# Performance work log

Hardware: AMD Instinct MI355X
Metric: run time of the kernel (lower is better)

The kernel has to match this reference:

```python
import jax, jax.numpy as jnp
import numpy as np

B, S, D = 2, 2048, 1024
NUM_HEAD = 8
HEAD_SIZE = D // NUM_HEAD


def setup_inputs() -> dict:
    key = jax.random.key(0)
    ks = jax.random.split(key, 10)
    scale = 1.0 / np.sqrt(D)
    inp = {
        "q": jax.random.normal(ks[0], (B, S, D), dtype=jnp.float32),
        "k": jax.random.normal(ks[1], (B, S, D), dtype=jnp.float32),
        "v": jax.random.normal(ks[2], (B, S, D), dtype=jnp.float32),
        "mask": jax.random.bernoulli(ks[3], 0.1, (B, 1, S, S)),
        "Wq": jax.random.normal(ks[4], (D, D), dtype=jnp.float32) * scale,
        "bq": jnp.zeros((D,), dtype=jnp.float32),
        "Wk": jax.random.normal(ks[5], (D, D), dtype=jnp.float32) * scale,
        "bk": jnp.zeros((D,), dtype=jnp.float32),
        "Wv": jax.random.normal(ks[6], (D, D), dtype=jnp.float32) * scale,
        "bv": jnp.zeros((D,), dtype=jnp.float32),
    }
    return inp


def _split_heads(x):
    # [B,S,D] -> [B,H,S,Hd]
    b, s, _ = x.shape
    return x.reshape(b, s, NUM_HEAD, HEAD_SIZE).transpose(0, 2, 1, 3)


def reference(q, k, v, mask, Wq, bq, Wk, bk, Wv, bv):
    Q = _split_heads(q @ Wq + bq)
    K = _split_heads(k @ Wk + bk)
    V = _split_heads(v @ Wv + bv)
    # scores [B,H,S,S]; NB: mask applied BEFORE scaling, as in the original
    QK = jnp.einsum("bhqd,bhkd->bhqk", Q, K)
    QK = jnp.where(mask, jnp.float32(-1e6), QK)
    QK = QK / jnp.float32(np.sqrt(HEAD_SIZE))
    attn = jax.nn.softmax(QK, axis=-1)  # dropout is identity in eval mode
    ctx = jnp.einsum("bhqk,bhkd->bhqd", attn, V)
    out = ctx.transpose(0, 2, 1, 3).reshape(q.shape[0], q.shape[1], D)
    return out
```

## Files before the change

kernel.cpp:

```cpp
#include <hip/hip_runtime.h>

typedef __bf16 bf16;
typedef __attribute__((ext_vector_type(8))) __bf16 bf16x8;
typedef __attribute__((ext_vector_type(4))) __bf16 bf16x4;
typedef __attribute__((ext_vector_type(4))) float f32x4;
typedef __attribute__((ext_vector_type(4))) float fvec4;

#define NB 2
#define SEQ 2048
#define DM 1024
#define NH 8
#define HD 128

#define QSCL (0.08838834764831845f * 1.4426950408889634f)

#define AS1 __attribute__((address_space(1)))
#define AS3 __attribute__((address_space(3)))

__global__ __launch_bounds__(256) void prep_kernel(
    const float* __restrict__ qi, const float* __restrict__ ki,
    const float* __restrict__ vi,
    const float* __restrict__ Wq, const float* __restrict__ Wk,
    const float* __restrict__ Wv,
    const unsigned int* __restrict__ mask32,
    bf16* __restrict__ Xc, bf16* __restrict__ Wt,
    unsigned int* __restrict__ flag)
{
    const int z   = blockIdx.y;
    const int tid = threadIdx.x;
    __shared__ __align__(16) bf16 tile[64][80];
    __shared__ unsigned int sred[256];

    if (z < 3) {
        const float* src = (z == 0) ? qi : (z == 1) ? ki : vi;
        bf16* dst = Xc + (size_t)z * ((size_t)NB * SEQ * DM);
        const size_t base = (size_t)blockIdx.x * 4096 + (size_t)tid * 16;
        fvec4 f[4];
        #pragma unroll
        for (int j = 0; j < 4; j++)
            f[j] = *(const fvec4*)(src + base + j * 4);
        bf16x8 h0, h1;
        #pragma unroll
        for (int e = 0; e < 8; e++) {
            h0[e] = (bf16)f[e >> 2][e & 3];
            h1[e] = (bf16)f[2 + (e >> 2)][e & 3];
        }
        *(bf16x8*)(dst + base)     = h0;
        *(bf16x8*)(dst + base + 8) = h1;
    } else if (z < 6) {
        if (blockIdx.x >= 256) return;
        const float* W = (z == 3) ? Wq : (z == 4) ? Wk : Wv;
        bf16* dst = Wt + (size_t)(z - 3) * ((size_t)DM * DM);
        const float scl = (z == 3) ? QSCL : 1.0f;
        const int n0 = (blockIdx.x & 15) * 64;
        const int k0 = (blockIdx.x >> 4) * 64;
        #pragma unroll
        for (int p = 0; p < 4; p++) {
            const int r = p * 16 + (tid >> 4);
            const int c = (tid & 15) * 4;
            const fvec4 wv = *(const fvec4*)(W + (size_t)(k0 + r) * DM + n0 + c);
            #pragma unroll
            for (int j = 0; j < 4; j++)
                tile[c + j][r] = (bf16)(wv[j] * scl);
        }
        __syncthreads();
        #pragma unroll
        for (int p = 0; p < 2; p++) {
            const int row = p * 32 + (tid >> 3);
            const int ch  = tid & 7;
            const bf16x8 hv = *(const bf16x8*)(&tile[row][ch * 8]);
            *(bf16x8*)(dst + (size_t)(n0 + row) * DM + k0 + ch * 8) = hv;
        }
    } else {
        if (blockIdx.x != 0) return;
        unsigned int f = 0;
        for (int i = tid; i < 1024; i += 256) {
            const unsigned int w2 = mask32[i];
            if ((w2 & 0xFEFEFEFEu) == 0u && (w2 & 0xFFFFFF00u) != 0u) f = 1;
        }
        sred[tid] = f;
        __syncthreads();
        if (tid == 0) {
            unsigned int r = 0;
            for (int i = 0; i < 256; i++) r |= sred[i];
            *flag = r;
        }
    }
}

__global__ __launch_bounds__(256) void proj_kernel(
    const bf16* __restrict__ Xc, const bf16* __restrict__ Wt,
    const float* __restrict__ bq, const float* __restrict__ bk,
    const float* __restrict__ bv,
    bf16* __restrict__ Qo, bf16* __restrict__ Ko, bf16* __restrict__ Vto,
    const void* __restrict__ mask, const unsigned int* __restrict__ flag,
    unsigned long long* __restrict__ bits)
{
    __shared__ __align__(16) bf16 As[2][128 * 64];
    __shared__ __align__(16) bf16 Bs[2][128 * 64];

    const int pz = blockIdx.z;
    const int tid = threadIdx.x;

    if (pz == 3) {
        const bool bytem = (*flag & 1u) != 0;
        const int wid = blockIdx.y * 8 + blockIdx.x;
        const int t   = wid * 256 + tid;
        unsigned short* const bits16o = (unsigned short*)bits;
        #pragma unroll 2
        for (int it = 0; it < 8; ++it) {
            const size_t e0 = ((size_t)it * 65536 + t) * 16;
            unsigned int b16 = 0;
            if (bytem) {
                const uint4 wv = *(const uint4*)((const unsigned char*)mask + e0);
                const unsigned int wd[4] = {wv.x, wv.y, wv.z, wv.w};
                #pragma unroll
                for (int j = 0; j < 4; j++) {
                    b16 |= ((wd[j] & 0x000000FFu) ? 1u : 0u) << (4 * j + 0);
                    b16 |= ((wd[j] & 0x0000FF00u) ? 1u : 0u) << (4 * j + 1);
                    b16 |= ((wd[j] & 0x00FF0000u) ? 1u : 0u) << (4 * j + 2);
                    b16 |= ((wd[j] & 0xFF000000u) ? 1u : 0u) << (4 * j + 3);
                }
            } else {
                const unsigned int* mw = (const unsigned int*)mask + e0;
                #pragma unroll
                for (int j = 0; j < 4; j++) {
                    const uint4 wv = *(const uint4*)(mw + 4 * j);
                    b16 |= (wv.x ? 1u : 0u) << (4 * j + 0);
                    b16 |= (wv.y ? 1u : 0u) << (4 * j + 1);
                    b16 |= (wv.z ? 1u : 0u) << (4 * j + 2);
                    b16 |= (wv.w ? 1u : 0u) << (4 * j + 3);
                }
            }
            bits16o[e0 >> 4] = (unsigned short)b16;
        }
        return;
    }

    const bf16* X  = Xc + (size_t)pz * ((size_t)NB * SEQ * DM);
    const bf16* Bt = Wt + (size_t)pz * ((size_t)DM * DM);
    const float* bias = (pz == 0) ? bq : (pz == 1) ? bk : bv;
    const float bscl  = (pz == 0) ? QSCL : 1.0f;
    bf16* dst = (pz == 0) ? Qo : (pz == 1) ? Ko : Vto;

    const int lane = tid & 63;
    const int w    = tid >> 6;
    const int q16  = lane >> 4;
    const int l15  = lane & 15;

    const int m0 = blockIdx.y * 128;
    const int n0 = blockIdx.x * 128;
    const int wm = (w >> 1) * 64;
    const int wn = (w & 1) * 64;

    auto stage = [&](int buf, int k0) {
        #pragma unroll
        for (int i = 0; i < 4; i++) {
            const int c   = i * 256 + tid;
            const int row = c >> 3;
            const int cir = c & 7;
            const bf16* src =
                X + (size_t)(m0 + row) * DM + k0 + ((cir ^ (row & 7)) << 3);
            __builtin_amdgcn_global_load_lds(
                (const AS1 void*)src,
                (AS3 void*)(&As[buf][c * 8]),
                16, 0, 0);
        }
        #pragma unroll
        for (int i = 0; i < 4; i++) {
            const int c   = i * 256 + tid;
            const int row = c >> 3;
            const int cir = c & 7;
            const bf16* src =
                Bt + (size_t)(n0 + row) * DM + k0 + ((cir ^ (row & 7)) << 3);
            __builtin_amdgcn_global_load_lds(
                (const AS1 void*)src,
                (AS3 void*)(&Bs[buf][c * 8]),
                16, 0, 0);
        }
    };

    f32x4 acc[4][4] = {};
    stage(0, 0);
    __syncthreads();
    int cur = 0;

    for (int kt = 0; kt < DM / 64; ++kt) {
        if (kt + 1 < DM / 64) stage(cur ^ 1, (kt + 1) * 64);
        const bf16* Asb = &As[cur][0];
        const bf16* Bsb = &Bs[cur][0];
        #pragma unroll
        for (int c2 = 0; c2 < 2; c2++) {
            bf16x8 af[4], bfr[4];
            #pragma unroll
            for (int mi = 0; mi < 4; mi++) {
                const int row = wm + mi * 16 + l15;
                af[mi] = *(const bf16x8*)(
                    Asb + row * 64 + (((c2 * 4 + q16) ^ (row & 7)) << 3));
            }
            #pragma unroll
            for (int ni = 0; ni < 4; ni++) {
                const int row = wn + ni * 16 + l15;
                bfr[ni] = *(const bf16x8*)(
                    Bsb + row * 64 + (((c2 * 4 + q16) ^ (row & 7)) << 3));
            }
            #pragma unroll
            for (int mi = 0; mi < 4; mi++)
                #pragma unroll
                for (int ni = 0; ni < 4; ni++)
                    acc[mi][ni] = __builtin_amdgcn_mfma_f32_16x16x32_bf16(
                        af[mi], bfr[ni], acc[mi][ni], 0, 0, 0);
        }
        __syncthreads();
        cur ^= 1;
    }

    float bias_v[4];
    #pragma unroll
    for (int ni = 0; ni < 4; ni++)
        bias_v[ni] = bias[n0 + wn + ni * 16 + l15];

    #pragma unroll
    for (int mi = 0; mi < 4; mi++) {
        #pragma unroll
        for (int ni = 0; ni < 4; ni++) {
            const int n  = n0 + wn + ni * 16 + l15;
            const int h  = n >> 7;
            const int hd = n & (HD - 1);
            #pragma unroll
            for (int r = 0; r < 4; r++) {
                const int m = m0 + wm + mi * 16 + q16 * 4 + r;
                const int b = m >> 11;
                const int s = m & (SEQ - 1);
                const float val = acc[mi][ni][r] + bias_v[ni] * bscl;
                size_t idx;
                if (pz == 2)
                    idx = ((size_t)(b * NH + h) * HD + hd) * SEQ + s;
                else
                    idx = ((size_t)(b * NH + h) * SEQ + s) * HD + hd;
                dst[idx] = (bf16)val;
            }
        }
    }
}

__global__ __launch_bounds__(256) void attn_kernel(
    const bf16* __restrict__ Q, const bf16* __restrict__ K,
    const bf16* __restrict__ Vt, const unsigned int* __restrict__ maskbits,
    float* __restrict__ out)
{
    __shared__ __align__(16) bf16 Ks[2][64 * 128];
    __shared__ __align__(16) bf16 Vs[2][128 * 64];
    __shared__ __align__(16) bf16 Ps[4][16 * 72];

    const int tid  = threadIdx.x;
    const int lane = tid & 63;
    const int w    = tid >> 6;
    const int q16  = lane >> 4;
    const int l15  = lane & 15;
    const int l3   = l15 & 7;

    const int b  = blockIdx.z;
    const int h  = blockIdx.y;
    const int q0 = blockIdx.x * 64;
    const int bh = b * NH + h;

    const bf16* Qb = Q  + (size_t)bh * SEQ * HD;
    const bf16* Kb = K  + (size_t)bh * SEQ * HD;
    const bf16* Vb = Vt + (size_t)bh * HD * SEQ;
    const unsigned long long* mb64 =
        (const unsigned long long*)maskbits + (size_t)b * (SEQ * SEQ / 64);
    const int qbase = q0 + w * 16 + q16 * 4;
    const unsigned long long* mrow = mb64 + (size_t)qbase * (SEQ / 64);

    const int qrow_a = q0 + w * 16 + l15;
    bf16x8 qf[4];
    #pragma unroll
    for (int c = 0; c < 4; c++)
        qf[c] = *(const bf16x8*)(Qb + (size_t)qrow_a * HD + c * 32 + q16 * 8);

    f32x4 o[8] = {};
    float m_i[4], l_i[4];
    #pragma unroll
    for (int r = 0; r < 4; r++) { m_i[r] = -__builtin_inff(); l_i[r] = 0.f; }

    const float MASKV = -1.0e6f * QSCL;

    auto stage = [&](int buf, int k0) {
        bf16* kd = &Ks[buf][0];
        bf16* vd = &Vs[buf][0];
        #pragma unroll
        for (int i = 0; i < 4; i++) {
            const int c   = i * 256 + tid;
            const int row = c >> 4;
            const int cir = c & 15;
            const bf16* src =
                Kb + (size_t)(k0 + row) * HD + ((cir ^ (row & 7)) << 3);
            __builtin_amdgcn_global_load_lds(
                (const AS1 void*)src,
                (AS3 void*)(kd + c * 8),
                16, 0, 0);
        }
        #pragma unroll
        for (int i = 0; i < 4; i++) {
            const int c   = i * 256 + tid;
            const int d   = c >> 3;
            const int cir = c & 7;
            const bf16* src =
                Vb + (size_t)d * SEQ + k0 + ((cir ^ (d & 7)) << 3);
            __builtin_amdgcn_global_load_lds(
                (const AS1 void*)src,
                (AS3 void*)(vd + c * 8),
                16, 0, 0);
        }
    };

    unsigned long long mwn[4];
    stage(0, 0);
    #pragma unroll
    for (int r = 0; r < 4; r++) mwn[r] = mrow[(size_t)r * (SEQ / 64)];
    __syncthreads();

    bf16* Pw = &Ps[w][0];
    int cur = 0;

    for (int kt = 0; kt < SEQ / 64; ++kt) {
        unsigned long long mw[4];
        #pragma unroll
        for (int r = 0; r < 4; r++) mw[r] = mwn[r];

        if (kt + 1 < SEQ / 64) stage(cur ^ 1, (kt + 1) * 64);
        const int ktn = (kt + 1) & (SEQ / 64 - 1);
        #pragma unroll
        for (int r = 0; r < 4; r++)
            mwn[r] = mrow[(size_t)r * (SEQ / 64) + ktn];

        const bf16* Ksb = &Ks[cur][0];
        const bf16* Vsb = &Vs[cur][0];

        f32x4 sf[4] = {};
        #pragma unroll
        for (int c = 0; c < 4; c++) {
            #pragma unroll
            for (int nf = 0; nf < 4; nf++) {
                const bf16x8 kf = *(const bf16x8*)(
                    Ksb + (nf * 16 + l15) * 128 + (((c * 4 + q16) ^ l3) << 3));
                sf[nf] = __builtin_amdgcn_mfma_f32_16x16x32_bf16(
                    qf[c], kf, sf[nf], 0, 0, 0);
            }
        }

        #pragma unroll
        for (int nf = 0; nf < 4; nf++)
            #pragma unroll
            for (int r = 0; r < 4; r++) {
                const int mk = (int)((mw[r] >> (nf * 16 + l15)) & 1ull);
                sf[nf][r] = mk ? MASKV : sf[nf][r];
            }

        float alpha[4];
        bool need = false;
        #pragma unroll
        for (int r = 0; r < 4; r++) {
            float mx = fmaxf(fmaxf(sf[0][r], sf[1][r]),
                             fmaxf(sf[2][r], sf[3][r]));
            #pragma unroll
            for (int off = 1; off < 16; off <<= 1)
                mx = fmaxf(mx, __shfl_xor(mx, off, 16));
            const float mnew = fmaxf(m_i[r], mx);
            alpha[r] = __builtin_amdgcn_exp2f(m_i[r] - mnew);
            need |= (mnew > m_i[r]);
            m_i[r] = mnew;
            float ps = 0.f;
            #pragma unroll
            for (int nf = 0; nf < 4; nf++) {
                const float p = __builtin_amdgcn_exp2f(sf[nf][r] - mnew);
                sf[nf][r] = p;
                ps += p;
            }
            l_i[r] = l_i[r] * alpha[r] + ps;
        }

        if (__ballot(need)) {
            #pragma unroll
            for (int df = 0; df < 8; df++)
                #pragma unroll
                for (int r = 0; r < 4; r++)
                    o[df][r] *= alpha[r];
        }

        #pragma unroll
        for (int nf = 0; nf < 4; nf++)
            #pragma unroll
            for (int r = 0; r < 4; r++)
                Pw[(q16 * 4 + r) * 72 + nf * 16 + l15] = (bf16)sf[nf][r];

        bf16x8 pf[2];
        #pragma unroll
        for (int cc = 0; cc < 2; cc++)
            pf[cc] = *(const bf16x8*)(Pw + l15 * 72 + cc * 32 + q16 * 8);

        #pragma unroll
        for (int df = 0; df < 8; df++) {
            #pragma unroll
            for (int cc = 0; cc < 2; cc++) {
                const bf16x8 vf = *(const bf16x8*)(
                    Vsb + (df * 16 + l15) * 64 + (((cc * 4 + q16) ^ l3) << 3));
                o[df] = __builtin_amdgcn_mfma_f32_16x16x32_bf16(
                    pf[cc], vf, o[df], 0, 0, 0);
            }
        }

        __syncthreads();
        cur ^= 1;
    }

    #pragma unroll
    for (int r = 0; r < 4; r++) {
        float ls = l_i[r];
        #pragma unroll
        for (int off = 1; off < 16; off <<= 1)
            ls += __shfl_xor(ls, off, 16);
        l_i[r] = 1.0f / ls;
    }
    #pragma unroll
    for (int df = 0; df < 8; df++) {
        #pragma unroll
        for (int r = 0; r < 4; r++) {
            const int qr = q0 + w * 16 + q16 * 4 + r;
            out[((size_t)b * SEQ + qr) * DM + h * HD + df * 16 + l15] =
                o[df][r] * l_i[r];
        }
    }
}

extern "C" void kernel_launch(void* const* d_in, const int* in_sizes, int n_in,
                              void* d_out, int out_size, void* d_ws, size_t ws_size,
                              hipStream_t stream) {
    const float* q    = (const float*)d_in[0];
    const float* k    = (const float*)d_in[1];
    const float* v    = (const float*)d_in[2];
    const void*  mask = d_in[3];
    const float* Wq   = (const float*)d_in[4];
    const float* bq   = (const float*)d_in[5];
    const float* Wk   = (const float*)d_in[6];
    const float* bk   = (const float*)d_in[7];
    const float* Wv   = (const float*)d_in[8];
    const float* bv   = (const float*)d_in[9];
    float* out = (float*)d_out;

    char* ws = (char*)d_ws;
    unsigned long long* bits = (unsigned long long*)ws;
    const size_t bits_bytes = (size_t)NB * SEQ * SEQ / 8;
    unsigned int* flag = (unsigned int*)(ws + bits_bytes);
    bf16* Qp = (bf16*)(ws + bits_bytes + 256);
    bf16* Kp = Qp + (size_t)NB * SEQ * DM;
    bf16* Vp = Kp + (size_t)NB * SEQ * DM;
    bf16* Xc = Vp + (size_t)NB * SEQ * DM;
    bf16* Wt = Xc + (size_t)3 * NB * SEQ * DM;

    prep_kernel<<<dim3(1024, 7), 256, 0, stream>>>(
        q, k, v, Wq, Wk, Wv, (const unsigned int*)mask, Xc, Wt, flag);

    dim3 pgrid(DM / 128, (NB * SEQ) / 128, 4);
    proj_kernel<<<pgrid, 256, 0, stream>>>(Xc, Wt, bq, bk, bv, Qp, Kp, Vp,
                                           mask, flag, bits);

    dim3 agrid(SEQ / 64, NH, NB);
    attn_kernel<<<agrid, 256, 0, stream>>>(Qp, Kp, Vp,
                                           (const unsigned int*)bits, out);
}
```

Before: 278.8 us.

## Process 32 query rows per wave in attention to reuse K/V fragments

Each wave now handles two 16-row query tiles (128 queries per block instead of 64), so every K and V fragment read from LDS feeds two MFMAs. This halves the K/V global-to-LDS traffic per query and the LDS reads per MFMA. The mask-word prefetch for the next tile is dropped, and masks are now loaded at the top of each iteration. Register pressure roughly doubles for accumulators, and the grid shrinks to 256 blocks, which may underfill the 256 CUs.

Measured after the change: 305.3 us. 9.5% more time.

```diff
diff --git a/kernel.cpp b/kernel.cpp
--- a/kernel.cpp
+++ b/kernel.cpp
@@ -251,7 +251,7 @@
 {
     __shared__ __align__(16) bf16 Ks[2][64 * 128];
     __shared__ __align__(16) bf16 Vs[2][128 * 64];
-    __shared__ __align__(16) bf16 Ps[4][16 * 72];
+    __shared__ __align__(16) bf16 Ps[4][32 * 72];
 
     const int tid  = threadIdx.x;
     const int lane = tid & 63;
@@ -262,27 +262,35 @@
 
     const int b  = blockIdx.z;
     const int h  = blockIdx.y;
-    const int q0 = blockIdx.x * 64;
+    const int q0 = blockIdx.x * 128;
     const int bh = b * NH + h;
+    const int wrow = w * 32;
 
     const bf16* Qb = Q  + (size_t)bh * SEQ * HD;
     const bf16* Kb = K  + (size_t)bh * SEQ * HD;
     const bf16* Vb = Vt + (size_t)bh * HD * SEQ;
     const unsigned long long* mb64 =
         (const unsigned long long*)maskbits + (size_t)b * (SEQ * SEQ / 64);
-    const int qbase = q0 + w * 16 + q16 * 4;
-    const unsigned long long* mrow = mb64 + (size_t)qbase * (SEQ / 64);
-
-    const int qrow_a = q0 + w * 16 + l15;
-    bf16x8 qf[4];
-    #pragma unroll
-    for (int c = 0; c < 4; c++)
-        qf[c] = *(const bf16x8*)(Qb + (size_t)qrow_a * HD + c * 32 + q16 * 8);
-
-    f32x4 o[8] = {};
-    float m_i[4], l_i[4];
-    #pragma unroll
-    for (int r = 0; r < 4; r++) { m_i[r] = -__builtin_inff(); l_i[r] = 0.f; }
+    const unsigned long long* mrow[2];
+    #pragma unroll
+    for (int mi = 0; mi < 2; mi++)
+        mrow[mi] = mb64 +
+            (size_t)(q0 + wrow + mi * 16 + q16 * 4) * (SEQ / 64);
+
+    bf16x8 qf[2][4];
+    #pragma unroll
+    for (int mi = 0; mi < 2; mi++)
+        #pragma unroll
+        for (int c = 0; c < 4; c++)
+            qf[mi][c] = *(const bf16x8*)(
+                Qb + (size_t)(q0 + wrow + mi * 16 + l15) * HD + c * 32 + q16 * 8);
+
+    f32x4 o[2][8] = {};
+    float m_i[2][4], l_i[2][4];
+    #pragma unroll
+    for (int mi = 0; mi < 2; mi++)
+        #pragma unroll
+        for (int r = 0; r < 4; r++) { m_i[mi][r] = -__builtin_inff(); l_i[mi][r] = 0.f; }
 
     const float MASKV = -1.0e6f * QSCL;
 
@@ -315,90 +323,100 @@
         }
     };
 
-    unsigned long long mwn[4];
     stage(0, 0);
-    #pragma unroll
-    for (int r = 0; r < 4; r++) mwn[r] = mrow[(size_t)r * (SEQ / 64)];
     __syncthreads();
 
     bf16* Pw = &Ps[w][0];
     int cur = 0;
 
     for (int kt = 0; kt < SEQ / 64; ++kt) {
-        unsigned long long mw[4];
-        #pragma unroll
-        for (int r = 0; r < 4; r++) mw[r] = mwn[r];
+        unsigned long long mw[2][4];
+        #pragma unroll
+        for (int mi = 0; mi < 2; mi++)
+            #pragma unroll
+            for (int r = 0; r < 4; r++)
+                mw[mi][r] = mrow[mi][(size_t)r * (SEQ / 64) + kt];
 
         if (kt + 1 < SEQ / 64) stage(cur ^ 1, (kt + 1) * 64);
-        const int ktn = (kt + 1) & (SEQ / 64 - 1);
-        #pragma unroll
-        for (int r = 0; r < 4; r++)
-            mwn[r] = mrow[(size_t)r * (SEQ / 64) + ktn];
 
         const bf16* Ksb = &Ks[cur][0];
         const bf16* Vsb = &Vs[cur][0];
 
-        f32x4 sf[4] = {};
+        f32x4 sf[2][4] = {};
         #pragma unroll
         for (int c = 0; c < 4; c++) {
             #pragma unroll
             for (int nf = 0; nf < 4; nf++) {
                 const bf16x8 kf = *(const bf16x8*)(
                     Ksb + (nf * 16 + l15) * 128 + (((c * 4 + q16) ^ l3) << 3));
-                sf[nf] = __builtin_amdgcn_mfma_f32_16x16x32_bf16(
-                    qf[c], kf, sf[nf], 0, 0, 0);
-            }
-        }
-
-        #pragma unroll
-        for (int nf = 0; nf < 4; nf++)
+                #pragma unroll
+                for (int mi = 0; mi < 2; mi++)
+                    sf[mi][nf] = __builtin_amdgcn_mfma_f32_16x16x32_bf16(
+                        qf[mi][c], kf, sf[mi][nf], 0, 0, 0);
+            }
+        }
+
+        #pragma unroll
+        for (int mi = 0; mi < 2; mi++)
+            #pragma unroll
+            for (int nf = 0; nf < 4; nf++)
+                #pragma unroll
+                for (int r = 0; r < 4; r++) {
+                    const int mk = (int)((mw[mi][r] >> (nf * 16 + l15)) & 1ull);
+                    sf[mi][nf][r] = mk ? MASKV : sf[mi][nf][r];
+                }
+
+        float alpha[2][4];
+        bool need = false;
+        #pragma unroll
+        for (int mi = 0; mi < 2; mi++)
             #pragma unroll
             for (int r = 0; r < 4; r++) {
-                const int mk = (int)((mw[r] >> (nf * 16 + l15)) & 1ull);
-                sf[nf][r] = mk ? MASKV : sf[nf][r];
-            }
-
-        float alpha[4];
-        bool need = false;
-        #pragma unroll
-        for (int r = 0; r < 4; r++) {
-            float mx = fmaxf(fmaxf(sf[0][r], sf[1][r]),
-                             fmaxf(sf[2][r], sf[3][r]));
-            #pragma unroll
-            for (int off = 1; off < 16; off <<= 1)
-                mx = fmaxf(mx, __shfl_xor(mx, off, 16));
-            const float mnew = fmaxf(m_i[r], mx);
-            alpha[r] = __builtin_amdgcn_exp2f(m_i[r] - mnew);
-            need |= (mnew > m_i[r]);
-            m_i[r] = mnew;
-            float ps = 0.f;
-            #pragma unroll
-            for (int nf = 0; nf < 4; nf++) {
-                const float p = __builtin_amdgcn_exp2f(sf[nf][r] - mnew);
-                sf[nf][r] = p;
-                ps += p;
-            }
-            l_i[r] = l_i[r] * alpha[r] + ps;
-        }
+                float mx = fmaxf(fmaxf(sf[mi][0][r], sf[mi][1][r]),
+                                 fmaxf(sf[mi][2][r], sf[mi][3][r]));
+                #pragma unroll
+                for (int off = 1; off < 16; off <<= 1)
+                    mx = fmaxf(mx, __shfl_xor(mx, off, 16));
+                const float mnew = fmaxf(m_i[mi][r], mx);
+                alpha[mi][r] = __builtin_amdgcn_exp2f(m_i[mi][r] - mnew);
+                need |= (mnew > m_i[mi][r]);
+                m_i[mi][r] = mnew;
+                float ps = 0.f;
+                #pragma unroll
+                for (int nf = 0; nf < 4; nf++) {
+                    const float p = __builtin_amdgcn_exp2f(sf[mi][nf][r] - mnew);
+                    sf[mi][nf][r] = p;
+                    ps += p;
+                }
+                l_i[mi][r] = l_i[mi][r] * alpha[mi][r] + ps;
+            }
 
         if (__ballot(need)) {
             #pragma unroll
-            for (int df = 0; df < 8; df++)
+            for (int mi = 0; mi < 2; mi++)
+                #pragma unroll
+                for (int df = 0; df < 8; df++)
+                    #pragma unroll
+                    for (int r = 0; r < 4; r++)
+                        o[mi][df][r] *= alpha[mi][r];
+        }
+
+        #pragma unroll
+        for (int mi = 0; mi < 2; mi++)
+            #pragma unroll
+            for (int nf = 0; nf < 4; nf++)
                 #pragma unroll
                 for (int r = 0; r < 4; r++)
-                    o[df][r] *= alpha[r];
-        }
-
-        #pragma unroll
-        for (int nf = 0; nf < 4; nf++)
-            #pragma unroll
-            for (int r = 0; r < 4; r++)
-                Pw[(q16 * 4 + r) * 72 + nf * 16 + l15] = (bf16)sf[nf][r];
-
-        bf16x8 pf[2];
-        #pragma unroll
-        for (int cc = 0; cc < 2; cc++)
-            pf[cc] = *(const bf16x8*)(Pw + l15 * 72 + cc * 32 + q16 * 8);
+                    Pw[(mi * 16 + q16 * 4 + r) * 72 + nf * 16 + l15] =
+                        (bf16)sf[mi][nf][r];
+
+        bf16x8 pf[2][2];
+        #pragma unroll
+        for (int mi = 0; mi < 2; mi++)
+            #pragma unroll
+            for (int cc = 0; cc < 2; cc++)
+                pf[mi][cc] = *(const bf16x8*)(
+                    Pw + (mi * 16 + l15) * 72 + cc * 32 + q16 * 8);
 
         #pragma unroll
         for (int df = 0; df < 8; df++) {
@@ -406,8 +424,10 @@
             for (int cc = 0; cc < 2; cc++) {
                 const bf16x8 vf = *(const bf16x8*)(
                     Vsb + (df * 16 + l15) * 64 + (((cc * 4 + q16) ^ l3) << 3));
-                o[df] = __builtin_amdgcn_mfma_f32_16x16x32_bf16(
-                    pf[cc], vf, o[df], 0, 0, 0);
+                #pragma unroll
+                for (int mi = 0; mi < 2; mi++)
+                    o[mi][df] = __builtin_amdgcn_mfma_f32_16x16x32_bf16(
+                        pf[mi][cc], vf, o[mi][df], 0, 0, 0);
             }
         }
 
@@ -416,22 +436,26 @@
     }
 
     #pragma unroll
-    for (int r = 0; r < 4; r++) {
-        float ls = l_i[r];
-        #pragma unroll
-        for (int off = 1; off < 16; off <<= 1)
-            ls += __shfl_xor(ls, off, 16);
-        l_i[r] = 1.0f / ls;
-    }
-    #pragma unroll
-    for (int df = 0; df < 8; df++) {
+    for (int mi = 0; mi < 2; mi++)
         #pragma unroll
         for (int r = 0; r < 4; r++) {
-            const int qr = q0 + w * 16 + q16 * 4 + r;
-            out[((size_t)b * SEQ + qr) * DM + h * HD + df * 16 + l15] =
-                o[df][r] * l_i[r];
-        }
-    }
+            float ls = l_i[mi][r];
+            #pragma unroll
+            for (int off = 1; off < 16; off <<= 1)
+                ls += __shfl_xor(ls, off, 16);
+            l_i[mi][r] = 1.0f / ls;
+        }
+    #pragma unroll
+    for (int mi = 0; mi < 2; mi++)
+        #pragma unroll
+        for (int df = 0; df < 8; df++) {
+            #pragma unroll
+            for (int r = 0; r < 4; r++) {
+                const int qr = q0 + wrow + mi * 16 + q16 * 4 + r;
+                out[((size_t)b * SEQ + qr) * DM + h * HD + df * 16 + l15] =
+                    o[mi][df][r] * l_i[mi][r];
+            }
+        }
 }
 
 extern "C" void kernel_launch(void* const* d_in, const int* in_sizes, int n_in,
@@ -466,7 +490,7 @@
     proj_kernel<<<pgrid, 256, 0, stream>>>(Xc, Wt, bq, bk, bv, Qp, Kp, Vp,
                                            mask, flag, bits);
 
-    dim3 agrid(SEQ / 64, NH, NB);
+    dim3 agrid(SEQ / 128, NH, NB);
     attn_kernel<<<agrid, 256, 0, stream>>>(Qp, Kp, Vp,
                                            (const unsigned int*)bits, out);
 }
```

## Swap MFMA operands so each lane owns one query row; add setprio

Applied to the files above, without the earlier changes.

Swaps the A/B operands of both MFMA chains so the accumulator is transposed and each lane holds a single query row. Softmax row max and sum then need only two cross-lane shuffles instead of four per row, with one running max/sum per lane and one 64-bit mask word load per lane instead of four. It also raises wave priority around the MFMA blocks. The P store into LDS and the output store change to the transposed layout, which alters LDS write and global store access patterns.

Result: faster. 267.9 us (-3.9%).

```diff
diff --git a/kernel.cpp b/kernel.cpp
--- a/kernel.cpp
+++ b/kernel.cpp
@@ -268,21 +268,20 @@
     const bf16* Qb = Q  + (size_t)bh * SEQ * HD;
     const bf16* Kb = K  + (size_t)bh * SEQ * HD;
     const bf16* Vb = Vt + (size_t)bh * HD * SEQ;
-    const unsigned long long* mb64 =
-        (const unsigned long long*)maskbits + (size_t)b * (SEQ * SEQ / 64);
-    const int qbase = q0 + w * 16 + q16 * 4;
-    const unsigned long long* mrow = mb64 + (size_t)qbase * (SEQ / 64);
-
-    const int qrow_a = q0 + w * 16 + l15;
+
+    const int q_l = q0 + w * 16 + l15;
+    const unsigned long long* mrowL =
+        (const unsigned long long*)maskbits + (size_t)b * (SEQ * SEQ / 64)
+        + (size_t)q_l * (SEQ / 64);
+
     bf16x8 qf[4];
     #pragma unroll
     for (int c = 0; c < 4; c++)
-        qf[c] = *(const bf16x8*)(Qb + (size_t)qrow_a * HD + c * 32 + q16 * 8);
+        qf[c] = *(const bf16x8*)(Qb + (size_t)q_l * HD + c * 32 + q16 * 8);
 
     f32x4 o[8] = {};
-    float m_i[4], l_i[4];
-    #pragma unroll
-    for (int r = 0; r < 4; r++) { m_i[r] = -__builtin_inff(); l_i[r] = 0.f; }
+    float m_l = -__builtin_inff();
+    float l_l = 0.f;
 
     const float MASKV = -1.0e6f * QSCL;
 
@@ -315,30 +314,24 @@
         }
     };
 
-    unsigned long long mwn[4];
     stage(0, 0);
-    #pragma unroll
-    for (int r = 0; r < 4; r++) mwn[r] = mrow[(size_t)r * (SEQ / 64)];
+    unsigned long long mwn = mrowL[0];
     __syncthreads();
 
     bf16* Pw = &Ps[w][0];
     int cur = 0;
 
     for (int kt = 0; kt < SEQ / 64; ++kt) {
-        unsigned long long mw[4];
-        #pragma unroll
-        for (int r = 0; r < 4; r++) mw[r] = mwn[r];
+        const unsigned long long mwv = mwn;
 
         if (kt + 1 < SEQ / 64) stage(cur ^ 1, (kt + 1) * 64);
-        const int ktn = (kt + 1) & (SEQ / 64 - 1);
-        #pragma unroll
-        for (int r = 0; r < 4; r++)
-            mwn[r] = mrow[(size_t)r * (SEQ / 64) + ktn];
+        mwn = mrowL[(kt + 1) & (SEQ / 64 - 1)];
 
         const bf16* Ksb = &Ks[cur][0];
         const bf16* Vsb = &Vs[cur][0];
 
         f32x4 sf[4] = {};
+        __builtin_amdgcn_s_setprio(1);
         #pragma unroll
         for (int c = 0; c < 4; c++) {
             #pragma unroll
@@ -346,60 +339,62 @@
                 const bf16x8 kf = *(const bf16x8*)(
                     Ksb + (nf * 16 + l15) * 128 + (((c * 4 + q16) ^ l3) << 3));
                 sf[nf] = __builtin_amdgcn_mfma_f32_16x16x32_bf16(
-                    qf[c], kf, sf[nf], 0, 0, 0);
-            }
-        }
+                    kf, qf[c], sf[nf], 0, 0, 0);
+            }
+        }
+        __builtin_amdgcn_s_setprio(0);
 
         #pragma unroll
         for (int nf = 0; nf < 4; nf++)
             #pragma unroll
             for (int r = 0; r < 4; r++) {
-                const int mk = (int)((mw[r] >> (nf * 16 + l15)) & 1ull);
+                const int mk = (int)((mwv >> (nf * 16 + q16 * 4 + r)) & 1ull);
                 sf[nf][r] = mk ? MASKV : sf[nf][r];
             }
 
-        float alpha[4];
-        bool need = false;
-        #pragma unroll
-        for (int r = 0; r < 4; r++) {
-            float mx = fmaxf(fmaxf(sf[0][r], sf[1][r]),
-                             fmaxf(sf[2][r], sf[3][r]));
-            #pragma unroll
-            for (int off = 1; off < 16; off <<= 1)
-                mx = fmaxf(mx, __shfl_xor(mx, off, 16));
-            const float mnew = fmaxf(m_i[r], mx);
-            alpha[r] = __builtin_amdgcn_exp2f(m_i[r] - mnew);
-            need |= (mnew > m_i[r]);
-            m_i[r] = mnew;
-            float ps = 0.f;
-            #pragma unroll
-            for (int nf = 0; nf < 4; nf++) {
+        float t0 = fmaxf(fmaxf(sf[0][0], sf[0][1]), fmaxf(sf[0][2], sf[0][3]));
+        float t1 = fmaxf(fmaxf(sf[1][0], sf[1][1]), fmaxf(sf[1][2], sf[1][3]));
+        float t2 = fmaxf(fmaxf(sf[2][0], sf[2][1]), fmaxf(sf[2][2], sf[2][3]));
+        float t3 = fmaxf(fmaxf(sf[3][0], sf[3][1]), fmaxf(sf[3][2], sf[3][3]));
+        float mx = fmaxf(fmaxf(t0, t1), fmaxf(t2, t3));
+        mx = fmaxf(mx, __shfl_xor(mx, 16));
+        mx = fmaxf(mx, __shfl_xor(mx, 32));
+        const float mnew  = fmaxf(m_l, mx);
+        const float alpha = __builtin_amdgcn_exp2f(m_l - mnew);
+        const bool  need  = mnew > m_l;
+        m_l = mnew;
+
+        float ps = 0.f;
+        #pragma unroll
+        for (int nf = 0; nf < 4; nf++)
+            #pragma unroll
+            for (int r = 0; r < 4; r++) {
                 const float p = __builtin_amdgcn_exp2f(sf[nf][r] - mnew);
                 sf[nf][r] = p;
                 ps += p;
             }
-            l_i[r] = l_i[r] * alpha[r] + ps;
-        }
+        l_l = l_l * alpha + ps;
 
         if (__ballot(need)) {
             #pragma unroll
             for (int df = 0; df < 8; df++)
                 #pragma unroll
                 for (int r = 0; r < 4; r++)
-                    o[df][r] *= alpha[r];
+                    o[df][r] *= alpha;
         }
 
         #pragma unroll
         for (int nf = 0; nf < 4; nf++)
             #pragma unroll
             for (int r = 0; r < 4; r++)
-                Pw[(q16 * 4 + r) * 72 + nf * 16 + l15] = (bf16)sf[nf][r];
+                Pw[l15 * 72 + nf * 16 + q16 * 4 + r] = (bf16)sf[nf][r];
 
         bf16x8 pf[2];
         #pragma unroll
         for (int cc = 0; cc < 2; cc++)
             pf[cc] = *(const bf16x8*)(Pw + l15 * 72 + cc * 32 + q16 * 8);
 
+        __builtin_amdgcn_s_setprio(1);
         #pragma unroll
         for (int df = 0; df < 8; df++) {
             #pragma unroll
@@ -407,29 +402,26 @@
                 const bf16x8 vf = *(const bf16x8*)(
                     Vsb + (df * 16 + l15) * 64 + (((cc * 4 + q16) ^ l3) << 3));
                 o[df] = __builtin_amdgcn_mfma_f32_16x16x32_bf16(
-                    pf[cc], vf, o[df], 0, 0, 0);
-            }
-        }
+                    vf, pf[cc], o[df], 0, 0, 0);
+            }
+        }
+        __builtin_amdgcn_s_setprio(0);
 
         __syncthreads();
         cur ^= 1;
     }
 
-    #pragma unroll
-    for (int r = 0; r < 4; r++) {
-        float ls = l_i[r];
-        #pragma unroll
-        for (int off = 1; off < 16; off <<= 1)
-            ls += __shfl_xor(ls, off, 16);
-        l_i[r] = 1.0f / ls;
-    }
+    float ls = l_l;
+    ls += __shfl_xor(ls, 16);
+    ls += __shfl_xor(ls, 32);
+    const float linv = 1.0f / ls;
+
     #pragma unroll
     for (int df = 0; df < 8; df++) {
         #pragma unroll
         for (int r = 0; r < 4; r++) {
-            const int qr = q0 + w * 16 + q16 * 4 + r;
-            out[((size_t)b * SEQ + qr) * DM + h * HD + df * 16 + l15] =
-                o[df][r] * l_i[r];
+            out[((size_t)b * SEQ + q_l) * DM + h * HD + df * 16 + q16 * 4 + r] =
+                o[df][r] * linv;
         }
     }
 }
```
